# Kernel optimization log

Measured on AMD Instinct MI355X. Metric: run time of the kernel, lower is better.

The kernel has to match this reference:

```python
import jax, jax.numpy as jnp
import numpy as np

N = 10000      # nodes
DEG = 8        # avg out-degree before symmetrization
B = 2          # batch
T = 8          # time steps
F_IN = 1
HID = 64       # spatial hidden = temporal hidden
K = 2          # power-conv hops


def setup_inputs() -> dict:
    rng = np.random.default_rng(0)
    # random sparse adjacency, symmetrized by concatenating reversed edges
    s0 = rng.integers(0, N, size=N * DEG)
    d0 = rng.integers(0, N, size=N * DEG)
    src = np.concatenate([s0, d0]).astype(np.int32)   # [E], E = 2*N*DEG
    dst = np.concatenate([d0, s0]).astype(np.int32)
    vals = np.ones(src.shape[0], np.float32)
    # symmetric normalization: A_hat = D^{-1/2} A D^{-1/2}
    deg = np.zeros(N, np.float32)
    np.add.at(deg, dst, vals)
    dinv = 1.0 / np.sqrt(np.maximum(deg, 1.0))
    vals = (dinv[src] * dinv[dst] * vals).astype(np.float32)

    key = jax.random.key(0)
    ks = jax.random.split(key, 12)
    sc = 0.05
    return {
        "x": jax.random.normal(ks[0], (B, N, T), jnp.float32),
        "edge_src": jnp.asarray(src),
        "edge_dst": jnp.asarray(dst),
        "edge_val": jnp.asarray(vals),
        # PowerGConvDyn layer 1: F_in -> HID, K+1 power weights
        "W_sp1": jax.random.normal(ks[1], (K + 1, F_IN, HID), jnp.float32) * sc,
        "b_sp1": jnp.zeros((HID,), jnp.float32),
        # PowerGConvDyn layer 2: HID -> HID
        "W_sp2": jax.random.normal(ks[2], (K + 1, HID, HID), jnp.float32) * sc,
        "b_sp2": jnp.zeros((HID,), jnp.float32),
        # GRU (torch layout: gates stacked r,z,n)
        "W_ih": jax.random.normal(ks[3], (3 * HID, HID), jnp.float32) * sc,
        "W_hh": jax.random.normal(ks[4], (3 * HID, HID), jnp.float32) * sc,
        "b_ih": jnp.zeros((3 * HID,), jnp.float32),
        "b_hh": jnp.zeros((3 * HID,), jnp.float32),
        # head
        "W_head": jax.random.normal(ks[5], (HID, 1), jnp.float32) * sc,
        "b_head": jnp.zeros((1,), jnp.float32),
    }


def reference(x, edge_src, edge_dst, edge_val,
              W_sp1, b_sp1, W_sp2, b_sp2,
              W_ih, W_hh, b_ih, b_hh, W_head, b_head):
    Bb, Nn, Tt = x.shape
    # batch all (b,t) slices as columns: [N, B*T, F_in]
    H = x.transpose(1, 0, 2).reshape(Nn, Bb * Tt, 1)

    def spmm(Z):  # A_hat @ Z on node axis; Z: [N, M, F]
        msgs = edge_val[:, None, None] * Z[edge_src]           # [E, M, F]
        return jax.ops.segment_sum(msgs, edge_dst, num_segments=Nn)

    def power_layer(Hin, W, b):  # out = sum_k (A^k H) W_k + b, then ReLU
        out = jnp.einsum('nmf,fo->nmo', Hin, W[0])
        Z = Hin
        for k in range(1, W.shape[0]):
            Z = spmm(Z)
            out = out + jnp.einsum('nmf,fo->nmo', Z, W[k])
        return jax.nn.relu(out + b)

    H = power_layer(H, W_sp1, b_sp1)   # [N, B*T, HID]
    H = power_layer(H, W_sp2, b_sp2)   # [N, B*T, HID]
    C = H.shape[-1]

    # [N, B*T, C] -> [T, B*N, C] sequences for the GRU
    Hs = H.reshape(Nn, Bb, Tt, C).transpose(2, 1, 0, 3).reshape(Tt, Bb * Nn, C)

    Hh = W_hh.shape[1]
    h0 = jnp.zeros((Bb * Nn, Hh), x.dtype)

    def gru_step(h, xt):
        gx = xt @ W_ih.T + b_ih
        gh = h @ W_hh.T + b_hh
        rx, zx, nx = jnp.split(gx, 3, axis=-1)
        rh, zh, nh = jnp.split(gh, 3, axis=-1)
        r = jax.nn.sigmoid(rx + rh)
        z = jax.nn.sigmoid(zx + zh)
        n = jnp.tanh(nx + r * nh)
        h = (1.0 - z) * n + z * h
        return h, None

    h_last, _ = jax.lax.scan(gru_step, h0, Hs)   # [B*N, HID]
    y = (h_last @ W_head + b_head).reshape(Bb, Nn)
    return y
```

## Files before the change

### kernel.cpp

```cpp
#include <hip/hip_runtime.h>
#include <math.h>

#define N_NODES 10000
#define B_SZ 2
#define T_STEPS 8
#define M_COLS 16
#define BN 20000
#define NM 160000

typedef __attribute__((ext_vector_type(8))) short short8;
typedef __attribute__((ext_vector_type(4))) float f32x4;

__device__ __forceinline__ float b2f(unsigned short u) {
  union { unsigned int i; float f; } x; x.i = ((unsigned int)u) << 16; return x.f;
}
__device__ __forceinline__ unsigned short f2b(float f) {
  unsigned int x = __float_as_uint(f);
  return (unsigned short)((x + 0x7fffu + ((x >> 16) & 1u)) >> 16);
}
__device__ __forceinline__ float sigm(float x) {
  return 1.f / (1.f + __expf(-x));
}
__device__ __forceinline__ float tanhfast(float x) {
  float xm = fmaxf(x, -15.f);
  float e = __expf(-2.f * xm);
  return (1.f - e) / (1.f + e);
}

__global__ __launch_bounds__(256) void k_count_prep(const int* __restrict__ dst, int* __restrict__ cnt, int E,
                                                    int eb,
                                                    const float* __restrict__ Wih, const float* __restrict__ W2,
                                                    const float* __restrict__ Whh,
                                                    unsigned short* __restrict__ Wbih,
                                                    unsigned short* __restrict__ W2t,
                                                    unsigned short* __restrict__ Whi,
                                                    unsigned short* __restrict__ Wlo) {
  if ((int)blockIdx.x < eb) {
    int e = blockIdx.x*256 + threadIdx.x;
    if (e < E) atomicAdd(&cnt[dst[e]], 1);
  } else {
    int i = (blockIdx.x - eb)*256 + threadIdx.x;
    if (i >= 12288) return;
    Wbih[i] = f2b(Wih[i]);
    int p = i >> 12, rem = i & 4095, c = rem >> 6, k = rem & 63;
    W2t[i] = f2b(W2[p*4096 + k*64 + c]);
    float v = Whh[i];
    unsigned short h = f2b(v);
    Whi[i] = h;
    Wlo[i] = f2b(v - b2f(h));
  }
}

__global__ __launch_bounds__(256) void k_scan(const int* __restrict__ cntin, int* __restrict__ rowp,
                                              int* __restrict__ cntz, int n) {
  const int K = 40;
  int t = threadIdx.x;
  int beg = t*K;
  int end = beg + K < n ? beg + K : n;
  int s = 0;
  for (int i = beg; i < end; ++i) s += cntin[i];
  int lane = t & 63, w = t >> 6;
  int v = s;
#pragma unroll
  for (int off = 1; off < 64; off <<= 1) {
    int u = __shfl_up(v, off, 64);
    if (lane >= off) v += u;
  }
  __shared__ int wsum[4];
  if (lane == 63) wsum[w] = v;
  __syncthreads();
  int woff = 0;
  for (int i = 0; i < w; ++i) woff += wsum[i];
  int run = woff + v - s;
  for (int i = beg; i < end; ++i) {
    rowp[i] = run;
    run += cntin[i];
    cntz[i] = 0;
  }
  if (t == 255) rowp[n] = run;
}

__global__ __launch_bounds__(256) void k_fill(const int* __restrict__ src, const int* __restrict__ dst,
                                              const float* __restrict__ val, const int* __restrict__ rowp,
                                              int* __restrict__ cur, int* __restrict__ csrs,
                                              float* __restrict__ csrv, int E) {
  int e = blockIdx.x*256 + threadIdx.x;
  if (e >= E) return;
  int d = dst[e];
  int p = atomicAdd(&cur[d], 1);
  int slot = rowp[d] + p;
  csrs[slot] = src[e];
  csrv[slot] = val[e];
}

__global__ __launch_bounds__(256) void k_spmmA(const float* __restrict__ x, float* __restrict__ Z1,
                                               const int* __restrict__ rowp, const int* __restrict__ csrs,
                                               const float* __restrict__ csrv) {
  int i = blockIdx.x*256 + threadIdx.x;
  int n = i >> 4, m = i & 15;
  int b = m >> 3, t = m & 7;
  int s = rowp[n], e = rowp[n+1];
  const float* xb = x + b*(N_NODES*T_STEPS) + t;
  float a0 = 0.f, a1 = 0.f;
  int k = s;
  for (; k + 1 < e; k += 2) {
    int s0 = csrs[k], s1 = csrs[k+1];
    float v0 = csrv[k], v1 = csrv[k+1];
    float x0 = xb[s0*T_STEPS], x1 = xb[s1*T_STEPS];
    a0 = fmaf(v0, x0, a0);
    a1 = fmaf(v1, x1, a1);
  }
  if (k < e) a0 = fmaf(csrv[k], xb[csrs[k]*T_STEPS], a0);
  Z1[i] = a0 + a1;
}

__global__ __launch_bounds__(256) void k_spmmB_l1(const float* __restrict__ x, const float* __restrict__ Z1,
                                                  const int* __restrict__ rowp, const int* __restrict__ csrs,
                                                  const float* __restrict__ csrv,
                                                  const float* __restrict__ W1, const float* __restrict__ b1,
                                                  unsigned short* __restrict__ H1b) {
  int i = blockIdx.x*256 + threadIdx.x;
  int n = i >> 4, m = i & 15;
  int b = m >> 3, t = m & 7;
  int s = rowp[n], e = rowp[n+1];
  float a0 = 0.f, a1 = 0.f;
  int k = s;
  for (; k + 1 < e; k += 2) {
    int s0 = csrs[k], s1 = csrs[k+1];
    float v0 = csrv[k], v1 = csrv[k+1];
    float z0g = Z1[s0*16 + m], z1g = Z1[s1*16 + m];
    a0 = fmaf(v0, z0g, a0);
    a1 = fmaf(v1, z1g, a1);
  }
  if (k < e) a0 = fmaf(csrv[k], Z1[csrs[k]*16 + m], a0);
  float z2 = a0 + a1;
  float z0 = x[b*(N_NODES*T_STEPS) + n*T_STEPS + t];
  float z1 = Z1[i];
  unsigned short* dst = H1b + (size_t)i*64;
  union { uint4 v; unsigned short s[8]; } o;
#pragma unroll
  for (int g = 0; g < 8; ++g) {
#pragma unroll
    for (int j = 0; j < 8; ++j) {
      int c = g*8 + j;
      float v = fmaf(z0, W1[c], fmaf(z1, W1[64+c], fmaf(z2, W1[128+c], b1[c])));
      o.s[j] = f2b(v > 0.f ? v : 0.f);
    }
    ((uint4*)dst)[g] = o.v;
  }
}

__global__ __launch_bounds__(256) void k_spmmC(const unsigned short* __restrict__ Zin,
                                               unsigned short* __restrict__ Zout,
                                               const int* __restrict__ rowp, const int* __restrict__ csrs,
                                               const float* __restrict__ csrv) {
  int c = blockIdx.x & 7;
  int grp = blockIdx.x >> 3;
  int n = grp*16 + (threadIdx.x >> 4);
  int l = threadIdx.x & 15;
  int off = c*128 + l*8;
  int s = rowp[n], e = rowp[n+1];
  float acc[8] = {0,0,0,0,0,0,0,0};
  int k = s;
  for (; k + 3 < e; k += 4) {
    int s0 = csrs[k], s1 = csrs[k+1], s2 = csrs[k+2], s3 = csrs[k+3];
    float v0 = csrv[k], v1 = csrv[k+1], v2 = csrv[k+2], v3 = csrv[k+3];
    union { uint4 u; unsigned short s[8]; } z0, z1, z2, z3;
    z0.u = *(const uint4*)(Zin + (size_t)s0*1024 + off);
    z1.u = *(const uint4*)(Zin + (size_t)s1*1024 + off);
    z2.u = *(const uint4*)(Zin + (size_t)s2*1024 + off);
    z3.u = *(const uint4*)(Zin + (size_t)s3*1024 + off);
#pragma unroll
    for (int j = 0; j < 8; ++j)
      acc[j] = fmaf(v3, b2f(z3.s[j]), fmaf(v2, b2f(z2.s[j]),
               fmaf(v1, b2f(z1.s[j]), fmaf(v0, b2f(z0.s[j]), acc[j]))));
  }
  for (; k < e; ++k) {
    int s0 = csrs[k];
    float v0 = csrv[k];
    union { uint4 u; unsigned short s[8]; } z0;
    z0.u = *(const uint4*)(Zin + (size_t)s0*1024 + off);
#pragma unroll
    for (int j = 0; j < 8; ++j) acc[j] = fmaf(v0, b2f(z0.s[j]), acc[j]);
  }
  union { uint4 u; unsigned short s[8]; } o;
#pragma unroll
  for (int j = 0; j < 8; ++j) o.s[j] = f2b(acc[j]);
  *(uint4*)(Zout + (size_t)n*1024 + off) = o.u;
}

__global__ __launch_bounds__(256) void k_layer2m(const unsigned short* __restrict__ H1b,
                                                 const unsigned short* __restrict__ Z1b,
                                                 const unsigned short* __restrict__ Z2b,
                                                 const unsigned short* __restrict__ Wt,
                                                 const float* __restrict__ b2,
                                                 unsigned short* __restrict__ OUT2b) {
  int wid = blockIdx.x*4 + (threadIdx.x >> 6);
  int lane = threadIdx.x & 63;
  int lr = lane & 15, hi = lane >> 4;
  int rowbase = wid*16;
  const short* A0 = (const short*)H1b + (size_t)(rowbase + lr)*64;
  const short* A1 = (const short*)Z1b + (size_t)(rowbase + lr)*64;
  const short* A2 = (const short*)Z2b + (size_t)(rowbase + lr)*64;
  short8 a[3][2];
  a[0][0] = *(const short8*)(A0 + hi*8); a[0][1] = *(const short8*)(A0 + 32 + hi*8);
  a[1][0] = *(const short8*)(A1 + hi*8); a[1][1] = *(const short8*)(A1 + 32 + hi*8);
  a[2][0] = *(const short8*)(A2 + hi*8); a[2][1] = *(const short8*)(A2 + 32 + hi*8);
  const short* Bp = (const short*)Wt;
  f32x4 acc[4];
#pragma unroll
  for (int ct = 0; ct < 4; ++ct) {
    int col = ct*16 + lr;
    f32x4 c = {0.f, 0.f, 0.f, 0.f};
#pragma unroll
    for (int p = 0; p < 3; ++p) {
      short8 b0 = *(const short8*)(Bp + p*4096 + col*64 + hi*8);
      short8 b1 = *(const short8*)(Bp + p*4096 + col*64 + 32 + hi*8);
      c = __builtin_amdgcn_mfma_f32_16x16x32_bf16(a[p][0], b0, c, 0, 0, 0);
      c = __builtin_amdgcn_mfma_f32_16x16x32_bf16(a[p][1], b1, c, 0, 0, 0);
    }
    acc[ct] = c;
  }
#pragma unroll
  for (int ct = 0; ct < 4; ++ct) {
    int col = ct*16 + lr;
    float bb = b2[col];
#pragma unroll
    for (int r = 0; r < 4; ++r) {
      int nm = rowbase + hi*4 + r;
      int n = nm >> 4, m = nm & 15;
      int bi = m >> 3, t = m & 7;
      float v = acc[ct][r] + bb;
      OUT2b[((size_t)((t*2 + bi)*N_NODES + n))*64 + col] = f2b(v > 0.f ? v : 0.f);
    }
  }
}

__global__ __launch_bounds__(256, 2) void k_gru(const unsigned short* __restrict__ OUT2b,
                                                const unsigned short* __restrict__ Whhi,
                                                const unsigned short* __restrict__ Whlo,
                                                const unsigned short* __restrict__ Wihb,
                                                const float* __restrict__ bih,
                                                const float* __restrict__ bhh,
                                                const float* __restrict__ Whead,
                                                const float* __restrict__ bhead,
                                                float* __restrict__ y) {
  extern __shared__ char smem[];
  uint4* WF = (uint4*)smem;
  float* HSb = (float*)(smem + 49152);
  int tid = threadIdx.x;
  for (int idx = tid; idx < 48*64; idx += 256) {
    int f = idx >> 6, ln = idx & 63;
    int lrr = ln & 15, h4r = ln >> 4;
    int g = (f < 24) ? f : f - 24;
    int ct = g >> 1, kc = g & 1;
    const unsigned short* src = (f < 24) ? Whhi : Whlo;
    WF[idx] = *(const uint4*)(src + (ct*16 + lrr)*64 + kc*32 + h4r*8);
  }
  int w = tid >> 6, lane = tid & 63;
  int lr = lane & 15, h4 = lane >> 4;
  float* hs = HSb + w*(16*68);
  for (int i = lane; i < 16*68; i += 64) hs[i] = 0.f;
  __syncthreads();
  int Wv = blockIdx.x*4 + w;
  if (Wv >= 1250) return;
  int base = Wv*16;
  int row0 = base + lr;
  int b0 = row0 >= N_NODES ? 1 : 0;
  int n0 = row0 - b0*N_NODES;

  float cR[4], cZ[4], bNi[4], bNh[4];
#pragma unroll
  for (int cr = 0; cr < 4; ++cr) {
    int col = cr*16 + lr;
    cR[cr]  = bih[col] + bhh[col];
    cZ[cr]  = bih[64+col] + bhh[64+col];
    bNi[cr] = bih[128+col];
    bNh[cr] = bhh[128+col];
  }
  float hreg[4][4];
#pragma unroll
  for (int cr = 0; cr < 4; ++cr)
#pragma unroll
    for (int j = 0; j < 4; ++j) hreg[cr][j] = 0.f;
  const short* O = (const short*)OUT2b;
  const short* Wx = (const short*)Wihb;

#pragma unroll 1
  for (int t = 0; t < 8; ++t) {
    short8 ax[2];
    size_t ab0 = ((size_t)((t*2 + b0)*N_NODES + n0))*64;
    ax[0] = *(const short8*)(O + ab0 + h4*8);
    ax[1] = *(const short8*)(O + ab0 + 32 + h4*8);
    short8 ahi[2], alo[2];
#pragma unroll
    for (int kc = 0; kc < 2; ++kc) {
      const float* hp = hs + lr*68 + kc*32 + h4*8;
      float4 v0 = *(const float4*)hp;
      float4 v1 = *(const float4*)(hp + 4);
      float hv[8];
      hv[0]=v0.x; hv[1]=v0.y; hv[2]=v0.z; hv[3]=v0.w;
      hv[4]=v1.x; hv[5]=v1.y; hv[6]=v1.z; hv[7]=v1.w;
      union { short8 v; unsigned short s[8]; } uh, ul;
#pragma unroll
      for (int j = 0; j < 8; ++j) {
        unsigned short hb = (unsigned short)(__float_as_uint(hv[j]) >> 16);
        uh.s[j] = hb;
        ul.s[j] = f2b(hv[j] - b2f(hb));
      }
      ahi[kc] = uh.v; alo[kc] = ul.v;
    }
    f32x4 aR[4], aZ[4], aNx[4], aNh[4];
#pragma unroll
    for (int cr = 0; cr < 4; ++cr) {
      f32x4 zz = {0.f,0.f,0.f,0.f};
      aR[cr] = zz; aZ[cr] = zz; aNx[cr] = zz; aNh[cr] = zz;
    }
#pragma unroll
    for (int g = 0; g < 6; ++g) {
      short8 fh[4], fl[4], fx[4];
#pragma unroll
      for (int p = 0; p < 4; ++p) {
        int pair = g*4 + p;
        fh[p] = *(const short8*)&WF[pair*64 + lane];
        fl[p] = *(const short8*)&WF[(24 + pair)*64 + lane];
        fx[p] = *(const short8*)(Wx + ((pair >> 1)*16 + lr)*64 + (pair & 1)*32 + h4*8);
      }
      __builtin_amdgcn_sched_barrier(0);
#pragma unroll
      for (int p = 0; p < 4; ++p) {
        int pair = g*4 + p;
        int ct = pair >> 1, kc = pair & 1;
        if (ct < 4) {
          aR[ct] = __builtin_amdgcn_mfma_f32_16x16x32_bf16(ax[kc],  fx[p], aR[ct], 0, 0, 0);
          aR[ct] = __builtin_amdgcn_mfma_f32_16x16x32_bf16(ahi[kc], fh[p], aR[ct], 0, 0, 0);
          aR[ct] = __builtin_amdgcn_mfma_f32_16x16x32_bf16(ahi[kc], fl[p], aR[ct], 0, 0, 0);
          aR[ct] = __builtin_amdgcn_mfma_f32_16x16x32_bf16(alo[kc], fh[p], aR[ct], 0, 0, 0);
        } else if (ct < 8) {
          int cc = ct - 4;
          aZ[cc] = __builtin_amdgcn_mfma_f32_16x16x32_bf16(ax[kc],  fx[p], aZ[cc], 0, 0, 0);
          aZ[cc] = __builtin_amdgcn_mfma_f32_16x16x32_bf16(ahi[kc], fh[p], aZ[cc], 0, 0, 0);
          aZ[cc] = __builtin_amdgcn_mfma_f32_16x16x32_bf16(ahi[kc], fl[p], aZ[cc], 0, 0, 0);
          aZ[cc] = __builtin_amdgcn_mfma_f32_16x16x32_bf16(alo[kc], fh[p], aZ[cc], 0, 0, 0);
        } else {
          int cc = ct - 8;
          aNx[cc] = __builtin_amdgcn_mfma_f32_16x16x32_bf16(ax[kc],  fx[p], aNx[cc], 0, 0, 0);
          aNh[cc] = __builtin_amdgcn_mfma_f32_16x16x32_bf16(ahi[kc], fh[p], aNh[cc], 0, 0, 0);
          aNh[cc] = __builtin_amdgcn_mfma_f32_16x16x32_bf16(ahi[kc], fl[p], aNh[cc], 0, 0, 0);
          aNh[cc] = __builtin_amdgcn_mfma_f32_16x16x32_bf16(alo[kc], fh[p], aNh[cc], 0, 0, 0);
        }
      }
    }
#pragma unroll
    for (int cr = 0; cr < 4; ++cr)
#pragma unroll
      for (int j = 0; j < 4; ++j) {
        float r = sigm(aR[cr][j] + cR[cr]);
        float z = sigm(aZ[cr][j] + cZ[cr]);
        float nn = tanhfast(aNx[cr][j] + bNi[cr] + r*(aNh[cr][j] + bNh[cr]));
        float hv = (1.f - z)*nn + z*hreg[cr][j];
        hreg[cr][j] = hv;
        hs[(h4*4 + j)*68 + cr*16 + lr] = hv;
      }
  }
  float wv[4];
#pragma unroll
  for (int cr = 0; cr < 4; ++cr) wv[cr] = Whead[cr*16 + lr];
#pragma unroll
  for (int j = 0; j < 4; ++j) {
    float p = 0.f;
#pragma unroll
    for (int cr = 0; cr < 4; ++cr) p = fmaf(hreg[cr][j], wv[cr], p);
    p += __shfl_xor(p, 1, 64);
    p += __shfl_xor(p, 2, 64);
    p += __shfl_xor(p, 4, 64);
    p += __shfl_xor(p, 8, 64);
    if (lr == 0) y[base + h4*4 + j] = p + bhead[0];
  }
}

extern "C" void kernel_launch(void* const* d_in, const int* in_sizes, int n_in,
                              void* d_out, int out_size, void* d_ws, size_t ws_size,
                              hipStream_t stream) {
  const float* x    = (const float*)d_in[0];
  const int*   esrc = (const int*)d_in[1];
  const int*   edst = (const int*)d_in[2];
  const float* eval = (const float*)d_in[3];
  const float* W1   = (const float*)d_in[4];
  const float* b1   = (const float*)d_in[5];
  const float* W2   = (const float*)d_in[6];
  const float* b2   = (const float*)d_in[7];
  const float* Wih  = (const float*)d_in[8];
  const float* Whh  = (const float*)d_in[9];
  const float* bih  = (const float*)d_in[10];
  const float* bhh  = (const float*)d_in[11];
  const float* Whead= (const float*)d_in[12];
  const float* bhead= (const float*)d_in[13];
  int E = in_sizes[1];
  float* y = (float*)d_out;

  char* wsb = (char*)d_ws;
  unsigned short* H1b   = (unsigned short*)(wsb + 0);
  unsigned short* ZB1   = (unsigned short*)(wsb + 20480000);
  unsigned short* ZB2   = (unsigned short*)(wsb + 40960000);
  unsigned short* OUT2b = (unsigned short*)(wsb + 61440000);
  float* Z1   = (float*)(wsb + 82560000);
  int*   rowp = (int*)(wsb + 83840000);
  int*   cnt  = (int*)(wsb + 83880064);
  int*   csrs = (int*)(wsb + 83920064);
  float* csrv = (float*)(wsb + 84560064);
  unsigned short* Wbih = (unsigned short*)(wsb + 85200064);
  unsigned short* W2t  = (unsigned short*)(wsb + 85224640);
  unsigned short* Whhi = (unsigned short*)(wsb + 85249280);
  unsigned short* Whlo = (unsigned short*)(wsb + 85273856);

  int eb = (E + 255) / 256;

  hipMemsetAsync(cnt, 0, N_NODES*sizeof(int), stream);
  k_count_prep<<<eb + 48, 256, 0, stream>>>(edst, cnt, E, eb, Wih, W2, Whh, Wbih, W2t, Whhi, Whlo);
  k_scan<<<1, 256, 0, stream>>>(cnt, rowp, cnt, N_NODES);
  k_fill<<<eb, 256, 0, stream>>>(esrc, edst, eval, rowp, cnt, csrs, csrv, E);

  k_spmmA<<<625, 256, 0, stream>>>(x, Z1, rowp, csrs, csrv);
  k_spmmB_l1<<<625, 256, 0, stream>>>(x, Z1, rowp, csrs, csrv, W1, b1, H1b);

  k_spmmC<<<5000, 256, 0, stream>>>(H1b, ZB1, rowp, csrs, csrv);
  k_spmmC<<<5000, 256, 0, stream>>>(ZB1, ZB2, rowp, csrs, csrv);
  k_layer2m<<<2500, 256, 0, stream>>>(H1b, ZB1, ZB2, W2t, b2, OUT2b);

  const int gru_lds = 49152 + 4*16*68*4;
  hipFuncSetAttribute((const void*)k_gru, hipFuncAttributeMaxDynamicSharedMemorySize, gru_lds);
  k_gru<<<313, 256, gru_lds, stream>>>(OUT2b, Whhi, Whlo, Wbih, bih, bhh, Whead, bhead, y);
}
```

Measured before the change: 232.1 us.

## Fuse second-hop SpMM with layer-2 MFMA projection via LDS staging

Merges the second k_spmmC pass and the k_layer2m matmul into one kernel. Each block gathers the A·Z1 rows for 16 nodes × 128 columns into shared memory, then runs the bf16 MFMA projection directly from LDS. This removes the ZB2 intermediate buffer's global write and read plus one kernel launch. In exchange each block now does a smaller GEMM slice (2 of the 16 m-columns) and reloads the weight tiles more often.

Measured after the change: 227.6 us. About the same (-1.9%).

```diff
diff --git a/kernel.cpp b/kernel.cpp
--- a/kernel.cpp
+++ b/kernel.cpp
@@ -189,49 +189,90 @@
   *(uint4*)(Zout + (size_t)n*1024 + off) = o.u;
 }
 
-__global__ __launch_bounds__(256) void k_layer2m(const unsigned short* __restrict__ H1b,
-                                                 const unsigned short* __restrict__ Z1b,
-                                                 const unsigned short* __restrict__ Z2b,
-                                                 const unsigned short* __restrict__ Wt,
-                                                 const float* __restrict__ b2,
-                                                 unsigned short* __restrict__ OUT2b) {
-  int wid = blockIdx.x*4 + (threadIdx.x >> 6);
-  int lane = threadIdx.x & 63;
-  int lr = lane & 15, hi = lane >> 4;
-  int rowbase = wid*16;
-  const short* A0 = (const short*)H1b + (size_t)(rowbase + lr)*64;
-  const short* A1 = (const short*)Z1b + (size_t)(rowbase + lr)*64;
-  const short* A2 = (const short*)Z2b + (size_t)(rowbase + lr)*64;
-  short8 a[3][2];
-  a[0][0] = *(const short8*)(A0 + hi*8); a[0][1] = *(const short8*)(A0 + 32 + hi*8);
-  a[1][0] = *(const short8*)(A1 + hi*8); a[1][1] = *(const short8*)(A1 + 32 + hi*8);
-  a[2][0] = *(const short8*)(A2 + hi*8); a[2][1] = *(const short8*)(A2 + 32 + hi*8);
+__global__ __launch_bounds__(256) void k_spmmC2_l2m(const unsigned short* __restrict__ H1b,
+                                                    const unsigned short* __restrict__ ZB1,
+                                                    const int* __restrict__ rowp, const int* __restrict__ csrs,
+                                                    const float* __restrict__ csrv,
+                                                    const unsigned short* __restrict__ Wt,
+                                                    const float* __restrict__ b2,
+                                                    unsigned short* __restrict__ OUT2b) {
+  __shared__ unsigned short Z2L[16][144];
+  int c = blockIdx.x & 7;
+  int grp = blockIdx.x >> 3;
+  int tid = threadIdx.x;
+  {
+    int ni = tid >> 4, l = tid & 15;
+    int n = grp*16 + ni;
+    int off = c*128 + l*8;
+    int s = rowp[n], e = rowp[n+1];
+    float acc[8] = {0,0,0,0,0,0,0,0};
+    int k = s;
+    for (; k + 3 < e; k += 4) {
+      int s0 = csrs[k], s1 = csrs[k+1], s2 = csrs[k+2], s3 = csrs[k+3];
+      float v0 = csrv[k], v1 = csrv[k+1], v2 = csrv[k+2], v3 = csrv[k+3];
+      union { uint4 u; unsigned short s[8]; } z0, z1, z2, z3;
+      z0.u = *(const uint4*)(ZB1 + (size_t)s0*1024 + off);
+      z1.u = *(const uint4*)(ZB1 + (size_t)s1*1024 + off);
+      z2.u = *(const uint4*)(ZB1 + (size_t)s2*1024 + off);
+      z3.u = *(const uint4*)(ZB1 + (size_t)s3*1024 + off);
+#pragma unroll
+      for (int j = 0; j < 8; ++j)
+        acc[j] = fmaf(v3, b2f(z3.s[j]), fmaf(v2, b2f(z2.s[j]),
+                 fmaf(v1, b2f(z1.s[j]), fmaf(v0, b2f(z0.s[j]), acc[j]))));
+    }
+    for (; k < e; ++k) {
+      int s0 = csrs[k];
+      float v0 = csrv[k];
+      union { uint4 u; unsigned short s[8]; } z0;
+      z0.u = *(const uint4*)(ZB1 + (size_t)s0*1024 + off);
+#pragma unroll
+      for (int j = 0; j < 8; ++j) acc[j] = fmaf(v0, b2f(z0.s[j]), acc[j]);
+    }
+    union { uint4 v; unsigned short s[8]; } o;
+#pragma unroll
+    for (int j = 0; j < 8; ++j) o.s[j] = f2b(acc[j]);
+    *(uint4*)&Z2L[ni][(l >> 3)*72 + (l & 7)*8] = o.v;
+  }
+  __syncthreads();
+  int w = tid >> 6, lane = tid & 63;
+  int lr = lane & 15, h4 = lane >> 4;
+  int q = w & 1, ch = w >> 1;
+  int m = 2*c + q;
+  short8 aH[2], aZ1[2], aZ2[2];
+#pragma unroll
+  for (int kc = 0; kc < 2; ++kc) {
+    size_t nm = ((size_t)(grp*16 + lr)*16 + m);
+    aH[kc]  = *(const short8*)((const short*)H1b + nm*64 + kc*32 + h4*8);
+    aZ1[kc] = *(const short8*)((const short*)ZB1 + nm*64 + kc*32 + h4*8);
+    aZ2[kc] = *(const short8*)&Z2L[lr][q*72 + kc*32 + h4*8];
+  }
   const short* Bp = (const short*)Wt;
-  f32x4 acc[4];
-#pragma unroll
-  for (int ct = 0; ct < 4; ++ct) {
-    int col = ct*16 + lr;
-    f32x4 c = {0.f, 0.f, 0.f, 0.f};
-#pragma unroll
-    for (int p = 0; p < 3; ++p) {
-      short8 b0 = *(const short8*)(Bp + p*4096 + col*64 + hi*8);
-      short8 b1 = *(const short8*)(Bp + p*4096 + col*64 + 32 + hi*8);
-      c = __builtin_amdgcn_mfma_f32_16x16x32_bf16(a[p][0], b0, c, 0, 0, 0);
-      c = __builtin_amdgcn_mfma_f32_16x16x32_bf16(a[p][1], b1, c, 0, 0, 0);
-    }
-    acc[ct] = c;
-  }
-#pragma unroll
-  for (int ct = 0; ct < 4; ++ct) {
-    int col = ct*16 + lr;
+  f32x4 accb[2];
+#pragma unroll
+  for (int ct2 = 0; ct2 < 2; ++ct2) {
+    int col = (ch*2 + ct2)*16 + lr;
+    f32x4 cc = {0.f, 0.f, 0.f, 0.f};
+#pragma unroll
+    for (int kc = 0; kc < 2; ++kc) {
+      short8 b0 = *(const short8*)(Bp + col*64 + kc*32 + h4*8);
+      short8 b1 = *(const short8*)(Bp + 4096 + col*64 + kc*32 + h4*8);
+      short8 b2f_ = *(const short8*)(Bp + 8192 + col*64 + kc*32 + h4*8);
+      cc = __builtin_amdgcn_mfma_f32_16x16x32_bf16(aH[kc],  b0,   cc, 0, 0, 0);
+      cc = __builtin_amdgcn_mfma_f32_16x16x32_bf16(aZ1[kc], b1,   cc, 0, 0, 0);
+      cc = __builtin_amdgcn_mfma_f32_16x16x32_bf16(aZ2[kc], b2f_, cc, 0, 0, 0);
+    }
+    accb[ct2] = cc;
+  }
+  int t = m & 7, bi = m >> 3;
+#pragma unroll
+  for (int ct2 = 0; ct2 < 2; ++ct2) {
+    int col = (ch*2 + ct2)*16 + lr;
     float bb = b2[col];
 #pragma unroll
     for (int r = 0; r < 4; ++r) {
-      int nm = rowbase + hi*4 + r;
-      int n = nm >> 4, m = nm & 15;
-      int bi = m >> 3, t = m & 7;
-      float v = acc[ct][r] + bb;
-      OUT2b[((size_t)((t*2 + bi)*N_NODES + n))*64 + col] = f2b(v > 0.f ? v : 0.f);
+      int n2 = grp*16 + h4*4 + r;
+      float v = accb[ct2][r] + bb;
+      OUT2b[((size_t)((t*2 + bi)*N_NODES + n2))*64 + col] = f2b(v > 0.f ? v : 0.f);
     }
   }
 }
@@ -402,7 +443,6 @@
   char* wsb = (char*)d_ws;
   unsigned short* H1b   = (unsigned short*)(wsb + 0);
   unsigned short* ZB1   = (unsigned short*)(wsb + 20480000);
-  unsigned short* ZB2   = (unsigned short*)(wsb + 40960000);
   unsigned short* OUT2b = (unsigned short*)(wsb + 61440000);
   float* Z1   = (float*)(wsb + 82560000);
   int*   rowp = (int*)(wsb + 83840000);
@@ -425,8 +465,7 @@
   k_spmmB_l1<<<625, 256, 0, stream>>>(x, Z1, rowp, csrs, csrv, W1, b1, H1b);
 
   k_spmmC<<<5000, 256, 0, stream>>>(H1b, ZB1, rowp, csrs, csrv);
-  k_spmmC<<<5000, 256, 0, stream>>>(ZB1, ZB2, rowp, csrs, csrv);
-  k_layer2m<<<2500, 256, 0, stream>>>(H1b, ZB1, ZB2, W2t, b2, OUT2b);
+  k_spmmC2_l2m<<<5000, 256, 0, stream>>>(H1b, ZB1, rowp, csrs, csrv, W2t, b2, OUT2b);
 
   const int gru_lds = 49152 + 4*16*68*4;
   hipFuncSetAttribute((const void*)k_gru, hipFuncAttributeMaxDynamicSharedMemorySize, gru_lds);
```
